# Optimization experiments

Hardware: AMD Instinct MI355X
Metric: run time of the kernel (lower is better)

Reference implementation:

```python
import jax, jax.numpy as jnp
import numpy as np

B, N, D, H = 2, 4096, 256, 8
HD = D // H
NEG_SLOPE = 0.01
LN_EPS = 1e-5


def setup_inputs() -> dict:
    key = jax.random.key(0)
    ks = jax.random.split(key, 6)
    s = 1.0 / np.sqrt(D)
    return {
        "h": jax.random.normal(ks[0], (B, N, D), dtype=jnp.float32),
        "W_l": jax.random.normal(ks[1], (D, D), dtype=jnp.float32) * s,
        "W_r": jax.random.normal(ks[2], (D, D), dtype=jnp.float32) * s,
        "a_l": jax.random.normal(ks[3], (HD,), dtype=jnp.float32) * s,
        "a_r": jax.random.normal(ks[4], (HD,), dtype=jnp.float32) * s,
        "W_final": jax.random.normal(ks[5], (D, D), dtype=jnp.float32) * s,
        "ln_g": jnp.ones((D,), dtype=jnp.float32),
        "ln_b": jnp.zeros((D,), dtype=jnp.float32),
    }


def _leaky(x):
    return jnp.where(x >= 0, x, NEG_SLOPE * x)


def reference(h, W_l, W_r, a_l, a_r, W_final, ln_g, ln_b):
    b, n, d = h.shape
    # projections -> [b, H, n, HD]
    fl = (h @ W_l).reshape(b, n, H, HD).transpose(0, 2, 1, 3)
    fr = (h @ W_r).reshape(b, n, H, HD).transpose(0, 2, 1, 3)
    # additive GAT-style scores: [b, H, n] each, broadcast to [b, H, n, n]
    sl = jnp.einsum("bhnd,d->bhn", _leaky(fl), a_l)
    sr = jnp.einsum("bhnd,d->bhn", _leaky(fr), a_r)
    score = sl[..., :, None] + sr[..., None, :]  # [b, H, n, n]
    attn = jnp.mean(score, axis=1)  # pre-softmax mean over heads: [b, n, n]
    p = jax.nn.softmax(score, axis=-1)  # dropout is identity (eval / p=0)
    context = jnp.einsum("bhij,bhjd->bhid", p, fr)  # [b, H, n, HD]
    h_sa = context.transpose(0, 2, 1, 3).reshape(b, n, d)
    fh = h_sa @ W_final
    x = h + fh
    mu = jnp.mean(x, axis=-1, keepdims=True)
    var = jnp.mean(jnp.square(x - mu), axis=-1, keepdims=True)
    h_out = (x - mu) * jax.lax.rsqrt(var + LN_EPS) * ln_g + ln_b
    return (h_out, attn)
```

## Files before the change

### kernel.cpp

```cpp
#include <hip/hip_runtime.h>
#include <hip/hip_bf16.h>

#define BATCH 2
#define SEQ   4096
#define DIM   256
#define HEADS 8
#define HDIM  32
#define M_ROWS (BATCH * SEQ)
#define JCHUNK 32
#define NCHUNK (SEQ / JCHUNK)
#define CTXBLKS (BATCH * NCHUNK)
#define FPSCALE 4294967296.0

typedef short bf16x8 __attribute__((ext_vector_type(8)));
typedef unsigned short u16x8 __attribute__((ext_vector_type(8)));
typedef float f32x4 __attribute__((ext_vector_type(4)));

static __device__ inline unsigned short f2bf(float x) {
  union { float f; unsigned u; } v; v.f = x;
  unsigned r = v.u + 0x7FFF + ((v.u >> 16) & 1);
  return (unsigned short)(r >> 16);
}

__global__ __launch_bounds__(256) void k_prep(const float* __restrict__ Wl,
                                              const float* __restrict__ Wr,
                                              unsigned short* __restrict__ Wt,
                                              unsigned long long* __restrict__ yacc,
                                              unsigned long long* __restrict__ wacc) {
  if (blockIdx.y == 0) {
    const int idx = blockIdx.x * 256 + threadIdx.x;
    yacc[2 * idx] = 0ull;
    yacc[2 * idx + 1] = 0ull;
    if (idx < BATCH * HEADS) wacc[idx] = 0ull;
  }
  __shared__ float tile[32][33];
  const int k0 = blockIdx.x * 32;
  const int n0 = blockIdx.y * 32;
  const int t = threadIdx.x;
  const float* W = (n0 < 256) ? Wl : Wr;
  const int nb = n0 & 255;
  {
    const int r = t >> 3;
    const int c = (t & 7) * 4;
    const float4 v = *(const float4*)(&W[(size_t)(k0 + r) * DIM + nb + c]);
    tile[r][c + 0] = v.x; tile[r][c + 1] = v.y;
    tile[r][c + 2] = v.z; tile[r][c + 3] = v.w;
  }
  __syncthreads();
  {
    const int nl = t >> 3;
    const int kl = (t & 7) * 4;
    ushort4 o;
    o.x = f2bf(tile[kl + 0][nl]); o.y = f2bf(tile[kl + 1][nl]);
    o.z = f2bf(tile[kl + 2][nl]); o.w = f2bf(tile[kl + 3][nl]);
    *(ushort4*)(&Wt[(size_t)(n0 + nl) * DIM + k0 + kl]) = o;
  }
}

__global__ __launch_bounds__(512) void k_gemm_fused(
    const float* __restrict__ A, const unsigned short* __restrict__ Wt,
    const float* __restrict__ a_l, const float* __restrict__ a_r,
    float* __restrict__ fr, float* __restrict__ sr,
    float* __restrict__ msl, float* __restrict__ msr) {
  __shared__ unsigned short As[64 * 32];
  __shared__ unsigned short Bs[256 * 32];
  __shared__ float red[64][8];

  const int bid = blockIdx.x;
  const int isR = bid & 1;
  const int bm  = bid >> 1;
  const int m0 = bm * 64;
  const int n0 = isR * 256;

  const int t = threadIdx.x;
  const int lane = t & 63;
  const int wid = t >> 6;

  f32x4 acc[4][2];
  #pragma unroll
  for (int i = 0; i < 4; ++i)
    #pragma unroll
    for (int j = 0; j < 2; ++j) acc[i][j] = (f32x4){0.f, 0.f, 0.f, 0.f};

  for (int k0 = 0; k0 < DIM; k0 += 32) {
    if (t < 256) {
      const int row = t >> 2;
      const int kc = t & 3;
      const int slot = kc ^ ((row >> 1) & 3);
      const float4 a0 = *(const float4*)(&A[(size_t)(m0 + row) * DIM + k0 + kc * 8]);
      const float4 a1 = *(const float4*)(&A[(size_t)(m0 + row) * DIM + k0 + kc * 8 + 4]);
      u16x8 pa;
      pa[0] = f2bf(a0.x); pa[1] = f2bf(a0.y); pa[2] = f2bf(a0.z); pa[3] = f2bf(a0.w);
      pa[4] = f2bf(a1.x); pa[5] = f2bf(a1.y); pa[6] = f2bf(a1.z); pa[7] = f2bf(a1.w);
      *(u16x8*)((char*)As + row * 64 + slot * 16) = pa;
    }
    #pragma unroll
    for (int p = 0; p < 2; ++p) {
      const int task = t + p * 512;
      const int row = task >> 2;
      const int kc = task & 3;
      const int slot = kc ^ ((row >> 1) & 3);
      const u16x8 pb = *(const u16x8*)(&Wt[(size_t)(n0 + row) * DIM + k0 + kc * 8]);
      *(u16x8*)((char*)Bs + row * 64 + slot * 16) = pb;
    }
    __syncthreads();

    bf16x8 af[4], bfr[2];
    #pragma unroll
    for (int mr = 0; mr < 4; ++mr) {
      const int ra = mr * 16 + (lane & 15);
      const int sl = (lane >> 4) ^ ((ra >> 1) & 3);
      af[mr] = *(const bf16x8*)((const char*)As + ra * 64 + sl * 16);
    }
    #pragma unroll
    for (int nr = 0; nr < 2; ++nr) {
      const int cb = wid * 32 + nr * 16 + (lane & 15);
      const int sl = (lane >> 4) ^ ((cb >> 1) & 3);
      bfr[nr] = *(const bf16x8*)((const char*)Bs + cb * 64 + sl * 16);
    }
    #pragma unroll
    for (int mr = 0; mr < 4; ++mr)
      #pragma unroll
      for (int nr = 0; nr < 2; ++nr)
        acc[mr][nr] = __builtin_amdgcn_mfma_f32_16x16x32_bf16(af[mr], bfr[nr], acc[mr][nr], 0, 0, 0);
    __syncthreads();
  }

  const float* av = isR ? a_r : a_l;
  const int b = m0 >> 12;
  const int nbase = m0 & 4095;

  #pragma unroll
  for (int mr = 0; mr < 4; ++mr) {
    #pragma unroll
    for (int r = 0; r < 4; ++r) {
      float p = 0.f;
      #pragma unroll
      for (int nr = 0; nr < 2; ++nr) {
        float x = acc[mr][nr][r];
        x = x >= 0.f ? x : 0.01f * x;
        p = fmaf(x, av[nr * 16 + (lane & 15)], p);
      }
      #pragma unroll
      for (int o = 1; o < 16; o <<= 1) p += __shfl_xor(p, o, 16);
      if ((lane & 15) == 0) {
        const int rl = mr * 16 + (lane >> 4) * 4 + r;
        red[rl][wid] = p;
        if (isR) sr[((size_t)(b * HEADS + wid)) * SEQ + nbase + rl] = p;
      }
    }
  }
  __syncthreads();
  if (t < 64) {
    float s = 0.f;
    #pragma unroll
    for (int h2 = 0; h2 < 8; ++h2) s += red[t][h2];
    (isR ? msr : msl)[m0 + t] = s * 0.125f;
  }
  if (isR) {
    #pragma unroll
    for (int mr = 0; mr < 4; ++mr)
      #pragma unroll
      for (int nr = 0; nr < 2; ++nr) {
        const int col = wid * 32 + nr * 16 + (lane & 15);
        #pragma unroll
        for (int r = 0; r < 4; ++r) {
          const int row = m0 + mr * 16 + (lane >> 4) * 4 + r;
          fr[(size_t)row * DIM + col] = acc[mr][nr][r];
        }
      }
  }
}

__global__ __launch_bounds__(256) void k_mega(const float* __restrict__ sr,
                                              const float* __restrict__ fr,
                                              const float* __restrict__ Wf,
                                              const float* __restrict__ msl,
                                              const float* __restrict__ msr,
                                              unsigned long long* __restrict__ yacc,
                                              unsigned long long* __restrict__ wacc,
                                              float* __restrict__ attn) {
  const int blk = blockIdx.x;
  const int t = threadIdx.x;

  if (blk < CTXBLKS) {
    __shared__ float ws_[HEADS][JCHUNK];
    __shared__ float cps[DIM];
    const int b  = blk >> 7;
    const int jc = blk & 127;
    const int j0 = jc * JCHUNK;
    {
      const int h2 = t >> 5, jj = t & 31;
      float e = expf(sr[((size_t)(b * HEADS + h2)) * SEQ + j0 + jj]);
      ws_[h2][jj] = e;
      float s = e;
      #pragma unroll
      for (int o = 16; o > 0; o >>= 1) s += __shfl_xor(s, o, 32);
      if (jj == 0)
        atomicAdd(&wacc[b * HEADS + h2],
                  (unsigned long long)__double2ll_rn((double)s * FPSCALE));
    }
    __syncthreads();
    {
      const int h2 = t >> 5;
      const float* frb = fr + (size_t)(b * SEQ + j0) * DIM + t;
      float accv = 0.f;
      #pragma unroll 8
      for (int jj = 0; jj < JCHUNK; ++jj)
        accv = fmaf(ws_[h2][jj], frb[(size_t)jj * DIM], accv);
      cps[t] = accv;
    }
    __syncthreads();
    #pragma unroll
    for (int h2 = 0; h2 < HEADS; ++h2) {
      float yh = 0.f;
      #pragma unroll 8
      for (int d = 0; d < HDIM; ++d)
        yh = fmaf(cps[h2 * HDIM + d], Wf[(size_t)(h2 * HDIM + d) * DIM + t], yh);
      atomicAdd(&yacc[(size_t)(b * HEADS + h2) * DIM + t],
                (unsigned long long)__double2ll_rn((double)yh * FPSCALE));
    }
  } else {
    const int pr = blk - CTXBLKS;
    const int row0 = pr * 2;
    const int b = row0 >> 12;
    const float v0 = msl[row0];
    const float v1 = msl[row0 + 1];
    const f32x4* mr4 = (const f32x4*)(msr + ((size_t)b << 12));
    f32x4* dst0 = (f32x4*)(attn + ((size_t)row0 << 12));
    f32x4* dst1 = (f32x4*)(attn + ((size_t)(row0 + 1) << 12));
    #pragma unroll
    for (int q = 0; q < 4; ++q) {
      const f32x4 m4 = mr4[q * 256 + t];
      __builtin_nontemporal_store(m4 + v0, &dst0[q * 256 + t]);
      __builtin_nontemporal_store(m4 + v1, &dst1[q * 256 + t]);
    }
  }
}

__global__ __launch_bounds__(256) void k_ln(const float* __restrict__ h,
                                            const unsigned long long* __restrict__ yacc,
                                            const unsigned long long* __restrict__ wacc,
                                            const float* __restrict__ g,
                                            const float* __restrict__ bb,
                                            float* __restrict__ out) {
  const int pr = blockIdx.x;
  const int row0 = pr * 2;
  const int b = row0 >> 12;
  const int t = threadIdx.x;

  float fh = 0.f;
  #pragma unroll
  for (int h2 = 0; h2 < HEADS; ++h2) {
    const double yv = (double)(long long)yacc[(size_t)(b * HEADS + h2) * DIM + t];
    const double wv = (double)(long long)wacc[b * HEADS + h2];
    fh += (float)(yv / wv);
  }

  const float x0 = h[(size_t)row0 * DIM + t] + fh;
  const float x1 = h[(size_t)(row0 + 1) * DIM + t] + fh;
  float s10 = x0, s20 = x0 * x0, s11 = x1, s21 = x1 * x1;
  #pragma unroll
  for (int o = 32; o > 0; o >>= 1) {
    s10 += __shfl_xor(s10, o, 64);
    s20 += __shfl_xor(s20, o, 64);
    s11 += __shfl_xor(s11, o, 64);
    s21 += __shfl_xor(s21, o, 64);
  }
  __shared__ float r1[2][4], r2[2][4];
  if ((t & 63) == 0) {
    r1[0][t >> 6] = s10; r2[0][t >> 6] = s20;
    r1[1][t >> 6] = s11; r2[1][t >> 6] = s21;
  }
  __syncthreads();
  const float gs = g[t], bs = bb[t];
  {
    const float s1 = r1[0][0] + r1[0][1] + r1[0][2] + r1[0][3];
    const float s2 = r2[0][0] + r2[0][1] + r2[0][2] + r2[0][3];
    const float mu = s1 * (1.f / 256.f);
    const float var = s2 * (1.f / 256.f) - mu * mu;
    const float rs = rsqrtf(var + 1e-5f);
    out[(size_t)row0 * DIM + t] = (x0 - mu) * rs * gs + bs;
  }
  {
    const float s1 = r1[1][0] + r1[1][1] + r1[1][2] + r1[1][3];
    const float s2 = r2[1][0] + r2[1][1] + r2[1][2] + r2[1][3];
    const float mu = s1 * (1.f / 256.f);
    const float var = s2 * (1.f / 256.f) - mu * mu;
    const float rs = rsqrtf(var + 1e-5f);
    out[(size_t)(row0 + 1) * DIM + t] = (x1 - mu) * rs * gs + bs;
  }
}

extern "C" void kernel_launch(void* const* d_in, const int* in_sizes, int n_in,
                              void* d_out, int out_size, void* d_ws, size_t ws_size,
                              hipStream_t stream) {
  const float* h  = (const float*)d_in[0];
  const float* Wl = (const float*)d_in[1];
  const float* Wr = (const float*)d_in[2];
  const float* al = (const float*)d_in[3];
  const float* ar = (const float*)d_in[4];
  const float* Wf = (const float*)d_in[5];
  const float* g  = (const float*)d_in[6];
  const float* bb = (const float*)d_in[7];
  float* out = (float*)d_out;

  unsigned long long* yacc = (unsigned long long*)d_ws;
  unsigned long long* wacc = yacc + BATCH * HEADS * DIM;
  float* fr  = (float*)(wacc + BATCH * HEADS);
  float* srs = fr + (size_t)M_ROWS * DIM;
  float* msl = srs + BATCH * HEADS * SEQ;
  float* msr = msl + M_ROWS;
  unsigned short* Wt = (unsigned short*)(msr + M_ROWS);

  k_prep<<<dim3(8, 16), 256, 0, stream>>>(Wl, Wr, Wt, yacc, wacc);
  k_gemm_fused<<<256, 512, 0, stream>>>(h, Wt, al, ar, fr, srs, msl, msr);
  k_mega<<<CTXBLKS + M_ROWS / 2, 256, 0, stream>>>(srs, fr, Wf, msl, msr,
                                                   yacc, wacc,
                                                   out + (size_t)M_ROWS * DIM);
  k_ln<<<M_ROWS / 2, 256, 0, stream>>>(h, yacc, wacc, g, bb, out);
}
```

Measured before the change: 68.53 us.

## Fuse softmax-weighted context reduction into projection GEMM epilogue and drop fr buffer

The exp weights and the weighted sum of fr over keys are now computed directly from the GEMM accumulators, using fixed-point atomics per batch and head. This removes the 8 MB fr store and reload and the sr round-trip. The per-head context is then multiplied by W_final in a tiny 2-block kernel, and the attn broadcast write is folded into the LayerNorm kernel. The costs are more atomics from the GEMM blocks, a small serial kernel, and __expf replacing expf.

```diff
diff --git a/kernel.cpp b/kernel.cpp
--- a/kernel.cpp
+++ b/kernel.cpp
@@ -7,9 +7,6 @@
 #define HEADS 8
 #define HDIM  32
 #define M_ROWS (BATCH * SEQ)
-#define JCHUNK 32
-#define NCHUNK (SEQ / JCHUNK)
-#define CTXBLKS (BATCH * NCHUNK)
 #define FPSCALE 4294967296.0
 
 typedef short bf16x8 __attribute__((ext_vector_type(8)));
@@ -25,12 +22,11 @@
 __global__ __launch_bounds__(256) void k_prep(const float* __restrict__ Wl,
                                               const float* __restrict__ Wr,
                                               unsigned short* __restrict__ Wt,
-                                              unsigned long long* __restrict__ yacc,
+                                              unsigned long long* __restrict__ yctx,
                                               unsigned long long* __restrict__ wacc) {
   if (blockIdx.y == 0) {
     const int idx = blockIdx.x * 256 + threadIdx.x;
-    yacc[2 * idx] = 0ull;
-    yacc[2 * idx + 1] = 0ull;
+    if (idx < BATCH * DIM) yctx[idx] = 0ull;
     if (idx < BATCH * HEADS) wacc[idx] = 0ull;
   }
   __shared__ float tile[32][33];
@@ -60,8 +56,9 @@
 __global__ __launch_bounds__(512) void k_gemm_fused(
     const float* __restrict__ A, const unsigned short* __restrict__ Wt,
     const float* __restrict__ a_l, const float* __restrict__ a_r,
-    float* __restrict__ fr, float* __restrict__ sr,
-    float* __restrict__ msl, float* __restrict__ msr) {
+    float* __restrict__ msl, float* __restrict__ msr,
+    unsigned long long* __restrict__ yctx,
+    unsigned long long* __restrict__ wacc) {
   __shared__ unsigned short As[64 * 32];
   __shared__ unsigned short Bs[256 * 32];
   __shared__ float red[64][8];
@@ -128,8 +125,8 @@
 
   const float* av = isR ? a_r : a_l;
   const int b = m0 >> 12;
-  const int nbase = m0 & 4095;
-
+
+  float e[4][4];
   #pragma unroll
   for (int mr = 0; mr < 4; ++mr) {
     #pragma unroll
@@ -146,8 +143,35 @@
       if ((lane & 15) == 0) {
         const int rl = mr * 16 + (lane >> 4) * 4 + r;
         red[rl][wid] = p;
-        if (isR) sr[((size_t)(b * HEADS + wid)) * SEQ + nbase + rl] = p;
       }
+      e[mr][r] = __expf(p) ;
+    }
+  }
+
+  if (isR) {
+    float se = 0.f;
+    #pragma unroll
+    for (int mr = 0; mr < 4; ++mr)
+      #pragma unroll
+      for (int r = 0; r < 4; ++r) se += e[mr][r];
+    se += __shfl_xor(se, 16, 64);
+    se += __shfl_xor(se, 32, 64);
+    if (lane == 0)
+      atomicAdd(&wacc[b * HEADS + wid],
+                (unsigned long long)__double2ll_rn((double)se * FPSCALE));
+    #pragma unroll
+    for (int nr = 0; nr < 2; ++nr) {
+      float y = 0.f;
+      #pragma unroll
+      for (int mr = 0; mr < 4; ++mr)
+        #pragma unroll
+        for (int r = 0; r < 4; ++r)
+          y = fmaf(e[mr][r], acc[mr][nr][r], y);
+      y += __shfl_xor(y, 16, 64);
+      y += __shfl_xor(y, 32, 64);
+      if (lane < 16)
+        atomicAdd(&yctx[(size_t)b * DIM + wid * 32 + nr * 16 + lane],
+                  (unsigned long long)__double2ll_rn((double)y * FPSCALE));
     }
   }
   __syncthreads();
@@ -157,106 +181,38 @@
     for (int h2 = 0; h2 < 8; ++h2) s += red[t][h2];
     (isR ? msr : msl)[m0 + t] = s * 0.125f;
   }
-  if (isR) {
-    #pragma unroll
-    for (int mr = 0; mr < 4; ++mr)
-      #pragma unroll
-      for (int nr = 0; nr < 2; ++nr) {
-        const int col = wid * 32 + nr * 16 + (lane & 15);
-        #pragma unroll
-        for (int r = 0; r < 4; ++r) {
-          const int row = m0 + mr * 16 + (lane >> 4) * 4 + r;
-          fr[(size_t)row * DIM + col] = acc[mr][nr][r];
-        }
-      }
-  }
-}
-
-__global__ __launch_bounds__(256) void k_mega(const float* __restrict__ sr,
-                                              const float* __restrict__ fr,
-                                              const float* __restrict__ Wf,
-                                              const float* __restrict__ msl,
-                                              const float* __restrict__ msr,
-                                              unsigned long long* __restrict__ yacc,
-                                              unsigned long long* __restrict__ wacc,
-                                              float* __restrict__ attn) {
-  const int blk = blockIdx.x;
-  const int t = threadIdx.x;
-
-  if (blk < CTXBLKS) {
-    __shared__ float ws_[HEADS][JCHUNK];
-    __shared__ float cps[DIM];
-    const int b  = blk >> 7;
-    const int jc = blk & 127;
-    const int j0 = jc * JCHUNK;
-    {
-      const int h2 = t >> 5, jj = t & 31;
-      float e = expf(sr[((size_t)(b * HEADS + h2)) * SEQ + j0 + jj]);
-      ws_[h2][jj] = e;
-      float s = e;
-      #pragma unroll
-      for (int o = 16; o > 0; o >>= 1) s += __shfl_xor(s, o, 32);
-      if (jj == 0)
-        atomicAdd(&wacc[b * HEADS + h2],
-                  (unsigned long long)__double2ll_rn((double)s * FPSCALE));
-    }
-    __syncthreads();
-    {
-      const int h2 = t >> 5;
-      const float* frb = fr + (size_t)(b * SEQ + j0) * DIM + t;
-      float accv = 0.f;
-      #pragma unroll 8
-      for (int jj = 0; jj < JCHUNK; ++jj)
-        accv = fmaf(ws_[h2][jj], frb[(size_t)jj * DIM], accv);
-      cps[t] = accv;
-    }
-    __syncthreads();
-    #pragma unroll
-    for (int h2 = 0; h2 < HEADS; ++h2) {
-      float yh = 0.f;
-      #pragma unroll 8
-      for (int d = 0; d < HDIM; ++d)
-        yh = fmaf(cps[h2 * HDIM + d], Wf[(size_t)(h2 * HDIM + d) * DIM + t], yh);
-      atomicAdd(&yacc[(size_t)(b * HEADS + h2) * DIM + t],
-                (unsigned long long)__double2ll_rn((double)yh * FPSCALE));
-    }
-  } else {
-    const int pr = blk - CTXBLKS;
-    const int row0 = pr * 2;
-    const int b = row0 >> 12;
-    const float v0 = msl[row0];
-    const float v1 = msl[row0 + 1];
-    const f32x4* mr4 = (const f32x4*)(msr + ((size_t)b << 12));
-    f32x4* dst0 = (f32x4*)(attn + ((size_t)row0 << 12));
-    f32x4* dst1 = (f32x4*)(attn + ((size_t)(row0 + 1) << 12));
-    #pragma unroll
-    for (int q = 0; q < 4; ++q) {
-      const f32x4 m4 = mr4[q * 256 + t];
-      __builtin_nontemporal_store(m4 + v0, &dst0[q * 256 + t]);
-      __builtin_nontemporal_store(m4 + v1, &dst1[q * 256 + t]);
-    }
-  }
-}
-
-__global__ __launch_bounds__(256) void k_ln(const float* __restrict__ h,
-                                            const unsigned long long* __restrict__ yacc,
+}
+
+__global__ __launch_bounds__(256) void k_fh(const unsigned long long* __restrict__ yctx,
                                             const unsigned long long* __restrict__ wacc,
-                                            const float* __restrict__ g,
-                                            const float* __restrict__ bb,
-                                            float* __restrict__ out) {
-  const int pr = blockIdx.x;
-  const int row0 = pr * 2;
+                                            const float* __restrict__ Wf,
+                                            float* __restrict__ fh2) {
+  const int b = blockIdx.x;
+  const int t = threadIdx.x;
+  __shared__ float c_s[DIM];
+  c_s[t] = (float)((double)(long long)yctx[(size_t)b * DIM + t] /
+                   (double)(long long)wacc[b * HEADS + (t >> 5)]);
+  __syncthreads();
+  float a2 = 0.f;
+  #pragma unroll 8
+  for (int k = 0; k < DIM; ++k)
+    a2 = fmaf(c_s[k], Wf[(size_t)k * DIM + t], a2);
+  fh2[b * DIM + t] = a2;
+}
+
+__global__ __launch_bounds__(256) void k_ln_attn(const float* __restrict__ h,
+                                                 const float* __restrict__ fh2,
+                                                 const float* __restrict__ g,
+                                                 const float* __restrict__ bb,
+                                                 const float* __restrict__ msl,
+                                                 const float* __restrict__ msr,
+                                                 float* __restrict__ out,
+                                                 float* __restrict__ attn) {
+  const int row0 = blockIdx.x * 2;
   const int b = row0 >> 12;
   const int t = threadIdx.x;
 
-  float fh = 0.f;
-  #pragma unroll
-  for (int h2 = 0; h2 < HEADS; ++h2) {
-    const double yv = (double)(long long)yacc[(size_t)(b * HEADS + h2) * DIM + t];
-    const double wv = (double)(long long)wacc[b * HEADS + h2];
-    fh += (float)(yv / wv);
-  }
-
+  const float fh = fh2[b * DIM + t];
   const float x0 = h[(size_t)row0 * DIM + t] + fh;
   const float x1 = h[(size_t)(row0 + 1) * DIM + t] + fh;
   float s10 = x0, s20 = x0 * x0, s11 = x1, s21 = x1 * x1;
@@ -289,6 +245,18 @@
     const float var = s2 * (1.f / 256.f) - mu * mu;
     const float rs = rsqrtf(var + 1e-5f);
     out[(size_t)(row0 + 1) * DIM + t] = (x1 - mu) * rs * gs + bs;
+  }
+
+  const float v0 = msl[row0];
+  const float v1 = msl[row0 + 1];
+  const f32x4* mr4 = (const f32x4*)(msr + ((size_t)b << 12));
+  f32x4* dst0 = (f32x4*)(attn + ((size_t)row0 << 12));
+  f32x4* dst1 = (f32x4*)(attn + ((size_t)(row0 + 1) << 12));
+  #pragma unroll
+  for (int q = 0; q < 4; ++q) {
+    const f32x4 m4 = mr4[q * 256 + t];
+    __builtin_nontemporal_store(m4 + v0, &dst0[q * 256 + t]);
+    __builtin_nontemporal_store(m4 + v1, &dst1[q * 256 + t]);
   }
 }
 
@@ -305,18 +273,16 @@
   const float* bb = (const float*)d_in[7];
   float* out = (float*)d_out;
 
-  unsigned long long* yacc = (unsigned long long*)d_ws;
-  unsigned long long* wacc = yacc + BATCH * HEADS * DIM;
-  float* fr  = (float*)(wacc + BATCH * HEADS);
-  float* srs = fr + (size_t)M_ROWS * DIM;
-  float* msl = srs + BATCH * HEADS * SEQ;
+  unsigned long long* yctx = (unsigned long long*)d_ws;
+  unsigned long long* wacc = yctx + BATCH * DIM;
+  float* msl = (float*)(wacc + BATCH * HEADS);
   float* msr = msl + M_ROWS;
-  unsigned short* Wt = (unsigned short*)(msr + M_ROWS);
-
-  k_prep<<<dim3(8, 16), 256, 0, stream>>>(Wl, Wr, Wt, yacc, wacc);
-  k_gemm_fused<<<256, 512, 0, stream>>>(h, Wt, al, ar, fr, srs, msl, msr);
-  k_mega<<<CTXBLKS + M_ROWS / 2, 256, 0, stream>>>(srs, fr, Wf, msl, msr,
-                                                   yacc, wacc,
-                                                   out + (size_t)M_ROWS * DIM);
-  k_ln<<<M_ROWS / 2, 256, 0, stream>>>(h, yacc, wacc, g, bb, out);
-}
+  float* fh2 = msr + M_ROWS;
+  unsigned short* Wt = (unsigned short*)(fh2 + BATCH * DIM);
+
+  k_prep<<<dim3(8, 16), 256, 0, stream>>>(Wl, Wr, Wt, yctx, wacc);
+  k_gemm_fused<<<256, 512, 0, stream>>>(h, Wt, al, ar, msl, msr, yctx, wacc);
+  k_fh<<<BATCH, 256, 0, stream>>>(yctx, wacc, Wf, fh2);
+  k_ln_attn<<<M_ROWS / 2, 256, 0, stream>>>(h, fh2, g, bb, msl, msr,
+                                            out, out + (size_t)M_ROWS * DIM);
+}
```

After: 57.05 us. 1.2x faster.
